# Kernel tuning notes

Hardware: AMD Instinct MI355X
Metric: run time of the kernel (lower is better)

## Reference

```python
import jax, jax.numpy as jnp
import numpy as np

N, B1, B2 = 16384, 1024, 64           # instances, level-1 bags, level-2 bags
C1, C2, K, P = 32, 64, 5, 2           # conv filters, kernel, pool size
D = 4 * 4 * C2                        # flatten dim: 28->24->12->8->4 spatial
ATT, CLS = 256, 512                   # attention units, classifier units


def _conv_relu(x, w, b):
    y = jax.lax.conv_general_dilated(
        x, w, window_strides=(1, 1), padding='VALID',
        dimension_numbers=('NHWC', 'HWIO', 'NHWC'))
    return jax.nn.relu(y + b)


def _maxpool(x):
    return jax.lax.reduce_window(
        x, -jnp.inf, jax.lax.max, (1, P, P, 1), (1, P, P, 1), 'VALID')


def _att_weights(emb, W, b, v, vb):
    # Dense(tanh) -> Dropout(identity at inference) -> Dense(1, sigmoid),
    # then GLOBAL softmax over all rows (softmax of the transposed [1,n] vector).
    h = jnp.tanh(emb @ W + b)
    s = jax.nn.sigmoid(h @ v + vb)     # [n, 1]
    return jax.nn.softmax(s[:, 0])     # [n], softmax across ALL rows


def setup_inputs() -> dict:
    key = jax.random.key(0)
    ks = jax.random.split(key, 12)

    def g(k, shape, scale=0.05):
        return scale * jax.random.normal(k, shape, dtype=jnp.float32)

    return {
        'x': jax.random.normal(ks[0], (N, 28, 28, 1), dtype=jnp.float32),
        'conv1_w': g(ks[1], (K, K, 1, C1)),
        'conv1_b': jnp.zeros((C1,), jnp.float32),
        'conv2_w': g(ks[2], (K, K, C1, C2)),
        'conv2_b': jnp.zeros((C2,), jnp.float32),
        'att1_W': g(ks[3], (D, ATT)), 'att1_b': jnp.zeros((ATT,), jnp.float32),
        'att1_v': g(ks[4], (ATT, 1)), 'att1_vb': jnp.zeros((1,), jnp.float32),
        'att2_W': g(ks[5], (D, ATT)), 'att2_b': jnp.zeros((ATT,), jnp.float32),
        'att2_v': g(ks[6], (ATT, 1)), 'att2_vb': jnp.zeros((1,), jnp.float32),
        'att3_W': g(ks[7], (D, ATT)), 'att3_b': jnp.zeros((ATT,), jnp.float32),
        'att3_v': g(ks[8], (ATT, 1)), 'att3_vb': jnp.zeros((1,), jnp.float32),
        'cls_W': g(ks[9], (D, CLS)), 'cls_b': jnp.zeros((CLS,), jnp.float32),
        'out_W': g(ks[10], (CLS, 1)), 'out_b': jnp.zeros((1,), jnp.float32),
        # sorted contiguous bag ids, every bag present (matches unique_with_counts loop)
        'first_lab': jnp.repeat(jnp.arange(B1, dtype=jnp.int32), N // B1),
        'second_lab': jnp.repeat(jnp.arange(B2, dtype=jnp.int32), B1 // B2),
    }


def reference(x, conv1_w, conv1_b, conv2_w, conv2_b,
              att1_W, att1_b, att1_v, att1_vb,
              att2_W, att2_b, att2_v, att2_vb,
              att3_W, att3_b, att3_v, att3_vb,
              cls_W, cls_b, out_W, out_b,
              first_lab, second_lab):
    h = _maxpool(_conv_relu(x, conv1_w, conv1_b))
    h = _maxpool(_conv_relu(h, conv2_w, conv2_b))       # [N, 4, 4, C2]
    emb1 = h.reshape(h.shape[0], -1)                    # [N, D]

    # level 1: attention-weighted bag pooling (instances -> B1 bags)
    w1 = _att_weights(emb1, att1_W, att1_b, att1_v, att1_vb)          # [N]
    emb2 = jax.ops.segment_sum(w1[:, None] * emb1, first_lab,
                               num_segments=B1)                       # [B1, D]

    # level 2: B1 bags -> B2 bags
    w2 = _att_weights(emb2, att2_W, att2_b, att2_v, att2_vb)          # [B1]
    emb3 = jax.ops.segment_sum(w2[:, None] * emb2, second_lab,
                               num_segments=B2)                       # [B2, D]

    # level 3: single outer bag over all B2 bags
    w3 = _att_weights(emb3, att3_W, att3_b, att3_v, att3_vb)          # [B2]
    outer = w3[None, :] @ emb3                                        # [1, D]

    pred = jax.nn.sigmoid((outer @ cls_W + cls_b) @ out_W + out_b)    # [1, 1]
    return pred
```

## Files before the change

### kernel.cpp

```cpp
#include <hip/hip_runtime.h>
#include <hip/hip_bf16.h>
#include <math.h>

typedef float f32x4 __attribute__((ext_vector_type(4)));
using bf16x8 = __attribute__((ext_vector_type(8))) short;
using f32x16 = __attribute__((ext_vector_type(16))) float;
typedef unsigned short ushortT;
using u16x4 = __attribute__((ext_vector_type(4))) unsigned short;

__device__ __forceinline__ ushortT f2bf(float f) {
  unsigned int u = __builtin_bit_cast(unsigned int, f);
  u = (u + 0x7FFFu + ((u >> 16) & 1u)) >> 16;
  return (ushortT)u;
}
__device__ __forceinline__ float bf2f(ushortT u) {
  return __builtin_bit_cast(float, (unsigned int)u << 16);
}
__device__ __forceinline__ void gload_lds16(const void* gsrc, void* ldst) {
  __builtin_amdgcn_global_load_lds(
      (const __attribute__((address_space(1))) unsigned int*)gsrc,
      (__attribute__((address_space(3))) unsigned int*)ldst, 16, 0, 0);
}

__global__ __launch_bounds__(256) void prepack_kernel(
    const float* __restrict__ w1, const float* __restrict__ w2,
    const float* __restrict__ aW1, const float* __restrict__ aW2,
    const float* __restrict__ aW3, const float* __restrict__ cls_W,
    const float* __restrict__ cls_b, const float* __restrict__ out_W,
    const float* __restrict__ out_b, ushortT* __restrict__ Bp1,
    ushortT* __restrict__ Bp2, ushortT* __restrict__ BpA1,
    ushortT* __restrict__ BpA2, ushortT* __restrict__ BpA3,
    float* __restrict__ u) {
  const int i = blockIdx.x * 256 + threadIdx.x;
  const int n1 = 1024, n2 = 51200, nA = 262144, nU = 65536;
  if (i < n1) {
    int nt = i >> 9, l = (i >> 3) & 63, j = i & 7;
    int tap = ((l >> 4) << 3) + j, ch = nt * 16 + (l & 15);
    Bp1[i] = (tap < 25) ? f2bf(w1[tap * 32 + ch]) : (ushortT)0;
  } else if (i < n1 + n2) {
    int t = i - n1;
    int co = t & 63, k = t >> 6;
    int s = k >> 4, hi = (k >> 3) & 1, j = k & 7;
    int nt = co >> 5, l31 = co & 31;
    Bp2[(s * 2 + nt) * 512 + (hi * 32 + l31) * 8 + j] = f2bf(w2[k * 64 + co]);
  } else if (i < n1 + n2 + 3 * nA) {
    int t = i - n1 - n2;
    int m = t >> 18, r = t & (nA - 1);
    const float* aW = (m == 0) ? aW1 : ((m == 1) ? aW2 : aW3);
    ushortT* dst = (m == 0) ? BpA1 : ((m == 1) ? BpA2 : BpA3);
    int col = r & 255, k = r >> 8;
    int nt = col >> 5, l31 = col & 31;
    int s = k >> 4, hi = (k >> 3) & 1, j = k & 7;
    dst[nt * 32768 + s * 512 + (hi * 32 + l31) * 8 + j] =
        f2bf(aW[k * 256 + col]);
  } else if (i < n1 + n2 + 3 * nA + nU) {
    int t = i - (n1 + n2 + 3 * nA);
    int k = t >> 6, lane = t & 63;
    float p = 0.f;
#pragma unroll
    for (int j = 0; j < 8; ++j) {
      int jj = lane + j * 64;
      p += cls_W[k * 512 + jj] * out_W[jj];
    }
#pragma unroll
    for (int off = 32; off; off >>= 1) p += __shfl_xor(p, off, 64);
    if (lane == 0) u[k] = p;
  } else if (i < n1 + n2 + 3 * nA + nU + 64) {
    int lane = i - (n1 + n2 + 3 * nA + nU);
    float p = 0.f;
#pragma unroll
    for (int j = 0; j < 8; ++j) {
      int jj = lane * 8 + j;
      p += cls_b[jj] * out_W[jj];
    }
#pragma unroll
    for (int off = 32; off; off >>= 1) p += __shfl_xor(p, off, 64);
    if (lane == 0) u[1024] = p + out_b[0];
  }
}

#define PADW 40
__global__ __launch_bounds__(256, 2) void fused_conv_mfma_kernel(
    const float* __restrict__ x, const ushortT* __restrict__ Bp1,
    const float* __restrict__ b1g, const ushortT* __restrict__ Bp2,
    const float* __restrict__ b2g, ushortT* __restrict__ emb1) {
  __shared__ ushortT xs[4][784];
  __shared__ ushortT h1s[4][144 * PADW];
  __shared__ ushortT Bbuf[2][4096];

  const int tid = threadIdx.x, wv = tid >> 6, lane = tid & 63;
  const int inst = blockIdx.x * 4 + wv;

  {
    int base = wv * 2048;
    gload_lds16((const char*)Bp2 + base + lane * 16, (char*)&Bbuf[0][0] + base);
    gload_lds16((const char*)Bp2 + base + 1024 + lane * 16,
                (char*)&Bbuf[0][0] + base + 1024);
  }

  const float* xg = x + (size_t)inst * 784;
  for (int i = lane; i < 784; i += 64) xs[wv][i] = f2bf(xg[i]);
  __syncthreads();

  {
    const int arow = lane & 15, kg = lane >> 4;
    int koff[8], kval[8];
#pragma unroll
    for (int j = 0; j < 8; ++j) {
      int tap = kg * 8 + j;
      int ky = (tap * 13) >> 6;
      int kx = tap - ky * 5;
      kval[j] = (tap < 25);
      koff[j] = kval[j] ? (ky * 28 + kx) : 0;
    }
    bf16x8 w1f0 = *(const bf16x8*)&Bp1[lane * 8];
    bf16x8 w1f1 = *(const bf16x8*)&Bp1[(64 + lane) * 8];
    const float bA = b1g[arow], bB = b1g[16 + arow];

#pragma unroll 4
    for (int g = 0; g < 36; ++g) {
      int R = g * 16 + arow;
      int q = R >> 2, quad = R & 3;
      int qy = q / 12, qx = q - qy * 12;
      int base = (2 * qy + (quad >> 1)) * 28 + 2 * qx + (quad & 1);
      bf16x8 a;
#pragma unroll
      for (int j = 0; j < 8; ++j) {
        ushortT vv = xs[wv][base + koff[j]];
        a[j] = (short)(kval[j] ? vv : (ushortT)0);
      }
      f32x4 c0, c1;
#pragma unroll
      for (int z = 0; z < 4; ++z) { c0[z] = 0.f; c1[z] = 0.f; }
      c0 = __builtin_amdgcn_mfma_f32_16x16x32_bf16(a, w1f0, c0, 0, 0, 0);
      c1 = __builtin_amdgcn_mfma_f32_16x16x32_bf16(a, w1f1, c1, 0, 0, 0);
      int qo = g * 4 + kg;
      float m0 = fmaxf(fmaxf(c0[0], c0[1]), fmaxf(c0[2], c0[3]));
      float m1 = fmaxf(fmaxf(c1[0], c1[1]), fmaxf(c1[2], c1[3]));
      h1s[wv][qo * PADW + arow] = f2bf(fmaxf(m0 + bA, 0.f));
      h1s[wv][qo * PADW + 16 + arow] = f2bf(fmaxf(m1 + bB, 0.f));
    }
  }
  __syncthreads();

  {
    const int hi = lane >> 5, l31 = lane & 31;
    int rowbase0, rowbase1;
    {
      int q2 = l31 >> 2, quad2 = l31 & 3;
      rowbase0 = (2 * (q2 >> 2) + (quad2 >> 1)) * 12 + 2 * (q2 & 3) + (quad2 & 1);
      q2 = (32 + l31) >> 2;
      rowbase1 = (2 * (q2 >> 2) + (quad2 >> 1)) * 12 + 2 * (q2 & 3) + (quad2 & 1);
    }
    const ushortT* h1w = &h1s[wv][0];

    f32x16 a00, a01, a10, a11;
#pragma unroll
    for (int z = 0; z < 16; ++z) { a00[z] = 0.f; a01[z] = 0.f; a10[z] = 0.f; a11[z] = 0.f; }

    for (int c = 0; c < 13; ++c) {
      if (c < 12) {
        char* dstb = (char*)&Bbuf[(c + 1) & 1][0];
        const char* srcb = (const char*)Bp2 + (size_t)(c + 1) * 8192;
        if (c + 1 < 12) {
          gload_lds16(srcb + wv * 2048 + lane * 16, dstb + wv * 2048);
          gload_lds16(srcb + wv * 2048 + 1024 + lane * 16,
                      dstb + wv * 2048 + 1024);
        } else {
          gload_lds16(srcb + wv * 1024 + lane * 16, dstb + wv * 1024);
        }
      }
      const ushortT* bb = &Bbuf[c & 1][0];
      const int ns = (c < 12) ? 4 : 2;
#pragma unroll
      for (int i = 0; i < 4; ++i) {
        if (i < ns) {
          int s = c * 4 + i;
          int tap = s >> 1;
          int ky = (tap * 13) >> 6, kx = tap - ky * 5;
          int aoff = (ky * 12 + kx) * PADW + ((s & 1) << 4) + hi * 8;
          bf16x8 bf0 = *(const bf16x8*)&bb[i * 1024 + lane * 8];
          bf16x8 bf1 = *(const bf16x8*)&bb[i * 1024 + 512 + lane * 8];
          bf16x8 af0 = *(const bf16x8*)&h1w[rowbase0 * PADW + aoff];
          bf16x8 af1 = *(const bf16x8*)&h1w[rowbase1 * PADW + aoff];
          a00 = __builtin_amdgcn_mfma_f32_32x32x16_bf16(af0, bf0, a00, 0, 0, 0);
          a01 = __builtin_amdgcn_mfma_f32_32x32x16_bf16(af0, bf1, a01, 0, 0, 0);
          a10 = __builtin_amdgcn_mfma_f32_32x32x16_bf16(af1, bf0, a10, 0, 0, 0);
          a11 = __builtin_amdgcn_mfma_f32_32x32x16_bf16(af1, bf1, a11, 0, 0, 0);
        }
      }
      __syncthreads();
    }

    const float b2_0 = b2g[l31], b2_1 = b2g[32 + l31];
    ushortT* erow = emb1 + (size_t)inst * 1024;
#pragma unroll
    for (int rg = 0; rg < 4; ++rg) {
      float m00 = fmaxf(fmaxf(a00[rg * 4], a00[rg * 4 + 1]),
                        fmaxf(a00[rg * 4 + 2], a00[rg * 4 + 3]));
      float m01 = fmaxf(fmaxf(a01[rg * 4], a01[rg * 4 + 1]),
                        fmaxf(a01[rg * 4 + 2], a01[rg * 4 + 3]));
      float m10 = fmaxf(fmaxf(a10[rg * 4], a10[rg * 4 + 1]),
                        fmaxf(a10[rg * 4 + 2], a10[rg * 4 + 3]));
      float m11 = fmaxf(fmaxf(a11[rg * 4], a11[rg * 4 + 1]),
                        fmaxf(a11[rg * 4 + 2], a11[rg * 4 + 3]));
      int p0 = 2 * rg + hi, p1 = 8 + 2 * rg + hi;
      erow[p0 * 64 + l31] = f2bf(fmaxf(m00 + b2_0, 0.f));
      erow[p0 * 64 + 32 + l31] = f2bf(fmaxf(m01 + b2_1, 0.f));
      erow[p1 * 64 + l31] = f2bf(fmaxf(m10 + b2_0, 0.f));
      erow[p1 * 64 + 32 + l31] = f2bf(fmaxf(m11 + b2_1, 0.f));
    }
  }
}

__device__ float att_rows32(const ushortT* __restrict__ emb_rm,
                            const ushortT* __restrict__ Bp,
                            const float* __restrict__ bias,
                            const float* __restrict__ v, float vb0, float invS,
                            float* wexp, float (*part)[4], float* esc) {
  const int tid = threadIdx.x, wv = tid >> 6, lane = tid & 63;
  const int hi = lane >> 5, l31 = lane & 31;
  const ushortT* ap = emb_rm + (size_t)l31 * 1024 + hi * 8;
  const ushortT* bp0 = Bp + (size_t)(2 * wv) * 32768 + (size_t)lane * 8;
  const ushortT* bp1 = bp0 + 32768;

  f32x16 a0, a1;
#pragma unroll
  for (int z = 0; z < 16; ++z) { a0[z] = 0.f; a1[z] = 0.f; }

#pragma unroll 8
  for (int s = 0; s < 64; ++s) {
    bf16x8 af = *(const bf16x8*)(ap + s * 16);
    bf16x8 b0 = *(const bf16x8*)(bp0 + s * 512);
    bf16x8 b1 = *(const bf16x8*)(bp1 + s * 512);
    a0 = __builtin_amdgcn_mfma_f32_32x32x16_bf16(af, b0, a0, 0, 0, 0);
    a1 = __builtin_amdgcn_mfma_f32_32x32x16_bf16(af, b1, a1, 0, 0, 0);
  }

  const int c0 = wv * 64 + l31, c1 = c0 + 32;
  const float bc0 = bias[c0], vc0 = v[c0];
  const float bc1 = bias[c1], vc1 = v[c1];
#pragma unroll
  for (int r = 0; r < 16; ++r) {
    float p = tanhf(a0[r] * invS + bc0) * vc0 + tanhf(a1[r] * invS + bc1) * vc1;
#pragma unroll
    for (int off = 16; off >= 1; off >>= 1) p += __shfl_xor(p, off, 64);
    if (l31 == 0) part[(r & 3) + 8 * (r >> 2) + 4 * hi][wv] = p;
  }
  __syncthreads();
  if (tid < 32) {
    float ss = vb0 + part[tid][0] + part[tid][1] + part[tid][2] + part[tid][3];
    float e = expf(1.f / (1.f + expf(-ss)));
    wexp[tid] = e;
#pragma unroll
    for (int off = 16; off >= 1; off >>= 1) e += __shfl_xor(e, off, 64);
    if (tid == 0) esc[0] = e;
  }
  __syncthreads();
  return esc[0];
}

__device__ void segsum_rm(const ushortT* __restrict__ emb_in,
                          const float* __restrict__ wexp,
                          ushortT* __restrict__ emb_out) {
  const int c4 = threadIdx.x * 4;
#pragma unroll
  for (int b = 0; b < 2; ++b) {
    f32x4 acc;
#pragma unroll
    for (int z = 0; z < 4; ++z) acc[z] = 0.f;
#pragma unroll
    for (int k = 0; k < 16; ++k) {
      u16x4 uu = *(const u16x4*)(emb_in + (size_t)(b * 16 + k) * 1024 + c4);
      float w = wexp[b * 16 + k];
      acc[0] += bf2f(uu[0]) * w;
      acc[1] += bf2f(uu[1]) * w;
      acc[2] += bf2f(uu[2]) * w;
      acc[3] += bf2f(uu[3]) * w;
    }
    u16x4 o;
#pragma unroll
    for (int z = 0; z < 4; ++z) o[z] = f2bf(acc[z]);
    *(u16x4*)(emb_out + (size_t)b * 1024 + c4) = o;
  }
}

__global__ __launch_bounds__(256, 2) void tail_kernel(
    const ushortT* __restrict__ emb1, const ushortT* __restrict__ BpA1,
    const ushortT* __restrict__ BpA2, const ushortT* __restrict__ BpA3,
    const float* __restrict__ a1b, const float* __restrict__ a1v,
    const float* __restrict__ a1vb, const float* __restrict__ a2b,
    const float* __restrict__ a2v, const float* __restrict__ a2vb,
    const float* __restrict__ a3b, const float* __restrict__ a3v,
    const float* __restrict__ a3vb, const float* __restrict__ u,
    ushortT* __restrict__ emb2u, ushortT* __restrict__ emb3u,
    unsigned* ctrl, float* __restrict__ out) {
  __shared__ float part[32][4];
  __shared__ float wexp[64];
  __shared__ float esc[1];
  __shared__ float Sv[2];
  __shared__ float redp[4];
  const int blk = blockIdx.x, tid = threadIdx.x;
  unsigned* ctr1 = ctrl;
  float* fs1 = (float*)(ctrl + 256);
  unsigned* ctr2 = ctrl + 512;
  float* fs2 = (float*)(ctrl + 768);

  float e1 = att_rows32(emb1 + (size_t)blk * 32768, BpA1, a1b, a1v, a1vb[0],
                        1.f, wexp, part, esc);
  segsum_rm(emb1 + (size_t)blk * 32768, wexp, emb2u + (size_t)blk * 2048);
  __syncthreads();
  if (tid == 0) {
    __threadfence();
    __hip_atomic_fetch_add(&fs1[(blk & 7) * 32], e1, __ATOMIC_RELAXED,
                           __HIP_MEMORY_SCOPE_AGENT);
    __hip_atomic_fetch_add(&ctr1[(blk & 7) * 32], 1u, __ATOMIC_RELEASE,
                           __HIP_MEMORY_SCOPE_AGENT);
  }
  if (blk >= 32) return;

  if (tid == 0) {
    unsigned t;
    do {
      t = 0;
      for (int i = 0; i < 8; ++i)
        t += __hip_atomic_load(&ctr1[i * 32], __ATOMIC_ACQUIRE,
                               __HIP_MEMORY_SCOPE_AGENT);
      if (t < 512) __builtin_amdgcn_s_sleep(2);
    } while (t < 512);
    __threadfence();
    float S = 0.f;
    for (int i = 0; i < 8; ++i)
      S += __hip_atomic_load(&fs1[i * 32], __ATOMIC_RELAXED,
                             __HIP_MEMORY_SCOPE_AGENT);
    Sv[0] = S;
  }
  __syncthreads();
  const float S1 = Sv[0];

  float e2 = att_rows32(emb2u + (size_t)blk * 32768, BpA2, a2b, a2v, a2vb[0],
                        1.f / S1, wexp, part, esc);
  segsum_rm(emb2u + (size_t)blk * 32768, wexp, emb3u + (size_t)blk * 2048);
  __syncthreads();
  if (tid == 0) {
    __threadfence();
    __hip_atomic_fetch_add(&fs2[(blk & 3) * 32], e2, __ATOMIC_RELAXED,
                           __HIP_MEMORY_SCOPE_AGENT);
    __hip_atomic_fetch_add(&ctr2[(blk & 3) * 32], 1u, __ATOMIC_RELEASE,
                           __HIP_MEMORY_SCOPE_AGENT);
  }
  if (blk >= 1) return;

  if (tid == 0) {
    unsigned t;
    do {
      t = 0;
      for (int i = 0; i < 4; ++i)
        t += __hip_atomic_load(&ctr2[i * 32], __ATOMIC_ACQUIRE,
                               __HIP_MEMORY_SCOPE_AGENT);
      if (t < 32) __builtin_amdgcn_s_sleep(2);
    } while (t < 32);
    __threadfence();
    float S = 0.f;
    for (int i = 0; i < 4; ++i)
      S += __hip_atomic_load(&fs2[i * 32], __ATOMIC_RELAXED,
                             __HIP_MEMORY_SCOPE_AGENT);
    Sv[1] = S;
  }
  __syncthreads();
  const float S2 = Sv[1];
  const float inv12 = 1.f / (S1 * S2);

  float ea = att_rows32(emb3u, BpA3, a3b, a3v, a3vb[0], inv12, wexp, part, esc);
  __syncthreads();
  float eb = att_rows32(emb3u + 32768, BpA3, a3b, a3v, a3vb[0], inv12,
                        wexp + 32, part, esc);
  __syncthreads();
  const float S3 = ea + eb;

  const int c4 = tid * 4;
  f32x4 outer;
#pragma unroll
  for (int z = 0; z < 4; ++z) outer[z] = 0.f;
#pragma unroll
  for (int b = 0; b < 64; ++b) {
    float w = wexp[b];
    u16x4 uu = *(const u16x4*)(emb3u + (size_t)b * 1024 + c4);
    outer[0] += bf2f(uu[0]) * w;
    outer[1] += bf2f(uu[1]) * w;
    outer[2] += bf2f(uu[2]) * w;
    outer[3] += bf2f(uu[3]) * w;
  }
  float zp = outer[0] * u[c4] + outer[1] * u[c4 + 1] + outer[2] * u[c4 + 2] +
             outer[3] * u[c4 + 3];
#pragma unroll
  for (int off = 32; off; off >>= 1) zp += __shfl_xor(zp, off, 64);
  if ((tid & 63) == 0) redp[tid >> 6] = zp;
  __syncthreads();
  if (tid == 0) {
    float z = (redp[0] + redp[1] + redp[2] + redp[3]) / (S1 * S2 * S3) +
              u[1024];
    out[0] = 1.f / (1.f + expf(-z));
  }
}

extern "C" void kernel_launch(void* const* d_in, const int* in_sizes, int n_in,
                              void* d_out, int out_size, void* d_ws,
                              size_t ws_size, hipStream_t stream) {
  const float* x       = (const float*)d_in[0];
  const float* conv1_w = (const float*)d_in[1];
  const float* conv1_b = (const float*)d_in[2];
  const float* conv2_w = (const float*)d_in[3];
  const float* conv2_b = (const float*)d_in[4];
  const float* att1_W  = (const float*)d_in[5];
  const float* att1_b  = (const float*)d_in[6];
  const float* att1_v  = (const float*)d_in[7];
  const float* att1_vb = (const float*)d_in[8];
  const float* att2_W  = (const float*)d_in[9];
  const float* att2_b  = (const float*)d_in[10];
  const float* att2_v  = (const float*)d_in[11];
  const float* att2_vb = (const float*)d_in[12];
  const float* att3_W  = (const float*)d_in[13];
  const float* att3_b  = (const float*)d_in[14];
  const float* att3_v  = (const float*)d_in[15];
  const float* att3_vb = (const float*)d_in[16];
  const float* cls_W   = (const float*)d_in[17];
  const float* cls_b   = (const float*)d_in[18];
  const float* out_W   = (const float*)d_in[19];
  const float* out_b   = (const float*)d_in[20];

  char* p = (char*)d_ws;
  unsigned* ctrl = (unsigned*)p; p += 4096;
  ushortT* emb1  = (ushortT*)p;  p += (size_t)16384 * 1024 * 2;
  ushortT* Bp1   = (ushortT*)p;  p += 2048;
  ushortT* Bp2   = (ushortT*)p;  p += 102400;
  ushortT* BpA1  = (ushortT*)p;  p += 524288;
  ushortT* BpA2  = (ushortT*)p;  p += 524288;
  ushortT* BpA3  = (ushortT*)p;  p += 524288;
  float* u       = (float*)p;    p += 8192;
  ushortT* emb2u = (ushortT*)p;  p += (size_t)1024 * 1024 * 2;
  ushortT* emb3u = (ushortT*)p;  p += 64 * 1024 * 2;

  prepack_kernel<<<3533, 256, 0, stream>>>(conv1_w, conv2_w, att1_W, att2_W,
                                           att3_W, cls_W, cls_b, out_W, out_b,
                                           Bp1, Bp2, BpA1, BpA2, BpA3, u);
  fused_conv_mfma_kernel<<<4096, 256, 0, stream>>>(x, Bp1, conv1_b, Bp2,
                                                   conv2_b, emb1);
  hipMemsetAsync(ctrl, 0, 4096, stream);
  tail_kernel<<<512, 256, 0, stream>>>(
      emb1, BpA1, BpA2, BpA3, att1_b, att1_v, att1_vb, att2_b, att2_v, att2_vb,
      att3_b, att3_v, att3_vb, u, emb2u, emb3u, ctrl, (float*)d_out);
}
```

Measured before the change: 453.1 us.

## Split fused tail kernel into three launches instead of spin-wait grid sync

Replaces the single tail kernel, which used atomic counters and spin-waiting blocks to order the three attention levels, with three separate launches whose ordering comes from the stream. Global softmax sums are accumulated with plain atomicAdd into a small buffer, zeroed earlier so the memset overlaps less with the tail. This removes the polling loops and fences and the idle resident blocks that waited on them. In exchange it pays two extra kernel launch gaps, and atomic float summation order becomes nondeterministic.

```diff
diff --git a/kernel.cpp b/kernel.cpp
--- a/kernel.cpp
+++ b/kernel.cpp
@@ -285,90 +285,48 @@
   }
 }
 
-__global__ __launch_bounds__(256, 2) void tail_kernel(
+__global__ __launch_bounds__(256, 2) void tailA_kernel(
     const ushortT* __restrict__ emb1, const ushortT* __restrict__ BpA1,
-    const ushortT* __restrict__ BpA2, const ushortT* __restrict__ BpA3,
     const float* __restrict__ a1b, const float* __restrict__ a1v,
-    const float* __restrict__ a1vb, const float* __restrict__ a2b,
-    const float* __restrict__ a2v, const float* __restrict__ a2vb,
+    const float* __restrict__ a1vb, ushortT* __restrict__ emb2u,
+    float* __restrict__ fs) {
+  __shared__ float part[32][4];
+  __shared__ float wexp[32];
+  __shared__ float esc[1];
+  const int blk = blockIdx.x;
+  float e1 = att_rows32(emb1 + (size_t)blk * 32768, BpA1, a1b, a1v, a1vb[0],
+                        1.f, wexp, part, esc);
+  segsum_rm(emb1 + (size_t)blk * 32768, wexp, emb2u + (size_t)blk * 2048);
+  if (threadIdx.x == 0) atomicAdd(&fs[0], e1);
+}
+
+__global__ __launch_bounds__(256, 2) void tailB_kernel(
+    const ushortT* __restrict__ emb2u, const ushortT* __restrict__ BpA2,
+    const float* __restrict__ a2b, const float* __restrict__ a2v,
+    const float* __restrict__ a2vb, const float* __restrict__ fs_in,
+    ushortT* __restrict__ emb3u, float* __restrict__ fs) {
+  __shared__ float part[32][4];
+  __shared__ float wexp[32];
+  __shared__ float esc[1];
+  const int blk = blockIdx.x;
+  float invS1 = 1.f / fs_in[0];
+  float e2 = att_rows32(emb2u + (size_t)blk * 32768, BpA2, a2b, a2v, a2vb[0],
+                        invS1, wexp, part, esc);
+  segsum_rm(emb2u + (size_t)blk * 32768, wexp, emb3u + (size_t)blk * 2048);
+  if (threadIdx.x == 0) atomicAdd(&fs[1], e2);
+}
+
+__global__ __launch_bounds__(256) void tailC_kernel(
+    const ushortT* __restrict__ emb3u, const ushortT* __restrict__ BpA3,
     const float* __restrict__ a3b, const float* __restrict__ a3v,
-    const float* __restrict__ a3vb, const float* __restrict__ u,
-    ushortT* __restrict__ emb2u, ushortT* __restrict__ emb3u,
-    unsigned* ctrl, float* __restrict__ out) {
+    const float* __restrict__ a3vb, const float* __restrict__ fs,
+    const float* __restrict__ u, float* __restrict__ out) {
   __shared__ float part[32][4];
   __shared__ float wexp[64];
   __shared__ float esc[1];
-  __shared__ float Sv[2];
   __shared__ float redp[4];
-  const int blk = blockIdx.x, tid = threadIdx.x;
-  unsigned* ctr1 = ctrl;
-  float* fs1 = (float*)(ctrl + 256);
-  unsigned* ctr2 = ctrl + 512;
-  float* fs2 = (float*)(ctrl + 768);
-
-  float e1 = att_rows32(emb1 + (size_t)blk * 32768, BpA1, a1b, a1v, a1vb[0],
-                        1.f, wexp, part, esc);
-  segsum_rm(emb1 + (size_t)blk * 32768, wexp, emb2u + (size_t)blk * 2048);
-  __syncthreads();
-  if (tid == 0) {
-    __threadfence();
-    __hip_atomic_fetch_add(&fs1[(blk & 7) * 32], e1, __ATOMIC_RELAXED,
-                           __HIP_MEMORY_SCOPE_AGENT);
-    __hip_atomic_fetch_add(&ctr1[(blk & 7) * 32], 1u, __ATOMIC_RELEASE,
-                           __HIP_MEMORY_SCOPE_AGENT);
-  }
-  if (blk >= 32) return;
-
-  if (tid == 0) {
-    unsigned t;
-    do {
-      t = 0;
-      for (int i = 0; i < 8; ++i)
-        t += __hip_atomic_load(&ctr1[i * 32], __ATOMIC_ACQUIRE,
-                               __HIP_MEMORY_SCOPE_AGENT);
-      if (t < 512) __builtin_amdgcn_s_sleep(2);
-    } while (t < 512);
-    __threadfence();
-    float S = 0.f;
-    for (int i = 0; i < 8; ++i)
-      S += __hip_atomic_load(&fs1[i * 32], __ATOMIC_RELAXED,
-                             __HIP_MEMORY_SCOPE_AGENT);
-    Sv[0] = S;
-  }
-  __syncthreads();
-  const float S1 = Sv[0];
-
-  float e2 = att_rows32(emb2u + (size_t)blk * 32768, BpA2, a2b, a2v, a2vb[0],
-                        1.f / S1, wexp, part, esc);
-  segsum_rm(emb2u + (size_t)blk * 32768, wexp, emb3u + (size_t)blk * 2048);
-  __syncthreads();
-  if (tid == 0) {
-    __threadfence();
-    __hip_atomic_fetch_add(&fs2[(blk & 3) * 32], e2, __ATOMIC_RELAXED,
-                           __HIP_MEMORY_SCOPE_AGENT);
-    __hip_atomic_fetch_add(&ctr2[(blk & 3) * 32], 1u, __ATOMIC_RELEASE,
-                           __HIP_MEMORY_SCOPE_AGENT);
-  }
-  if (blk >= 1) return;
-
-  if (tid == 0) {
-    unsigned t;
-    do {
-      t = 0;
-      for (int i = 0; i < 4; ++i)
-        t += __hip_atomic_load(&ctr2[i * 32], __ATOMIC_ACQUIRE,
-                               __HIP_MEMORY_SCOPE_AGENT);
-      if (t < 32) __builtin_amdgcn_s_sleep(2);
-    } while (t < 32);
-    __threadfence();
-    float S = 0.f;
-    for (int i = 0; i < 4; ++i)
-      S += __hip_atomic_load(&fs2[i * 32], __ATOMIC_RELAXED,
-                             __HIP_MEMORY_SCOPE_AGENT);
-    Sv[1] = S;
-  }
-  __syncthreads();
-  const float S2 = Sv[1];
+  const int tid = threadIdx.x;
+  const float S1 = fs[0], S2 = fs[1];
   const float inv12 = 1.f / (S1 * S2);
 
   float ea = att_rows32(emb3u, BpA3, a3b, a3v, a3vb[0], inv12, wexp, part, esc);
@@ -430,7 +388,7 @@
   const float* out_b   = (const float*)d_in[20];
 
   char* p = (char*)d_ws;
-  unsigned* ctrl = (unsigned*)p; p += 4096;
+  float* fs      = (float*)p;    p += 256;
   ushortT* emb1  = (ushortT*)p;  p += (size_t)16384 * 1024 * 2;
   ushortT* Bp1   = (ushortT*)p;  p += 2048;
   ushortT* Bp2   = (ushortT*)p;  p += 102400;
@@ -444,10 +402,13 @@
   prepack_kernel<<<3533, 256, 0, stream>>>(conv1_w, conv2_w, att1_W, att2_W,
                                            att3_W, cls_W, cls_b, out_W, out_b,
                                            Bp1, Bp2, BpA1, BpA2, BpA3, u);
+  hipMemsetAsync(fs, 0, 256, stream);
   fused_conv_mfma_kernel<<<4096, 256, 0, stream>>>(x, Bp1, conv1_b, Bp2,
                                                    conv2_b, emb1);
-  hipMemsetAsync(ctrl, 0, 4096, stream);
-  tail_kernel<<<512, 256, 0, stream>>>(
-      emb1, BpA1, BpA2, BpA3, att1_b, att1_v, att1_vb, att2_b, att2_v, att2_vb,
-      att3_b, att3_v, att3_vb, u, emb2u, emb3u, ctrl, (float*)d_out);
-}
+  tailA_kernel<<<512, 256, 0, stream>>>(emb1, BpA1, att1_b, att1_v, att1_vb,
+                                        emb2u, fs);
+  tailB_kernel<<<32, 256, 0, stream>>>(emb2u, BpA2, att2_b, att2_v, att2_vb,
+                                       fs, emb3u, fs);
+  tailC_kernel<<<1, 256, 0, stream>>>(emb3u, BpA3, att3_b, att3_v, att3_vb,
+                                      fs, u, (float*)d_out);
+}
```

Measured after the change: 393.2 us. 1.15x faster.
